# Kernel tuning notes

Measured on AMD Instinct MI355X. Metric: run time of the kernel, lower is better.

The kernel has to match this reference:

```python
import jax, jax.numpy as jnp
import numpy as np

B, S, H, L, NH, DH, FF = 64, 256, 768, 12, 12, 64, 3072
V, MAXP, NTYPE, NI, NS = 30522, 512, 2, 10, 64


def setup_inputs() -> dict:
    key = jax.random.key(0)
    ks = iter(jax.random.split(key, 40))
    n = lambda shp, s=0.02: jax.random.normal(next(ks), shp, jnp.float32) * s
    inp = {
        'input_ids': jax.random.randint(next(ks), (B, S), 0, V),
        'attention_mask': jnp.ones((B, S), jnp.int32),
        'token_type_ids': jnp.zeros((B, S), jnp.int32),
        'intent_labels': jax.random.randint(next(ks), (B,), 0, NI),
        'slot_labels': jax.random.randint(next(ks), (B, S), 0, NS),
        'word_emb': n((V, H)), 'pos_emb': n((MAXP, H)), 'type_emb': n((NTYPE, H)),
        'emb_ln_g': jnp.ones((H,)), 'emb_ln_b': jnp.zeros((H,)),
        'Wq': n((L, H, H)), 'bq': jnp.zeros((L, H)),
        'Wk': n((L, H, H)), 'bk': jnp.zeros((L, H)),
        'Wv': n((L, H, H)), 'bv': jnp.zeros((L, H)),
        'Wo': n((L, H, H)), 'bo': jnp.zeros((L, H)),
        'ln1_g': jnp.ones((L, H)), 'ln1_b': jnp.zeros((L, H)),
        'W1': n((L, H, FF)), 'b1': jnp.zeros((L, FF)),
        'W2': n((L, FF, H)), 'b2': jnp.zeros((L, H)),
        'ln2_g': jnp.ones((L, H)), 'ln2_b': jnp.zeros((L, H)),
        'Wi': n((H, NI)), 'bi': jnp.zeros((NI,)),
        'Ws': n((H, NS)), 'bs': jnp.zeros((NS,)),
        'crf_start': n((NS,), 0.1), 'crf_end': n((NS,), 0.1),
        'crf_trans': n((NS, NS), 0.1),
    }
    return inp


def _ln(x, g, b):
    m = x.mean(-1, keepdims=True)
    v = jnp.square(x - m).mean(-1, keepdims=True)
    return (x - m) * jax.lax.rsqrt(v + 1e-12) * g + b


def _forward(params, input_ids, attention_mask, token_type_ids, intent_labels, slot_labels):
    (word_emb, pos_emb, type_emb, emb_ln_g, emb_ln_b,
     Wq, bq, Wk, bk, Wv, bv, Wo, bo, ln1_g, ln1_b,
     W1, b1, W2, b2, ln2_g, ln2_b,
     Wi, bi, Ws, bs, crf_start, crf_end, crf_trans) = params
    Bn, Sn = input_ids.shape
    Hn = word_emb.shape[1]
    dh = Hn // NH
    # BERT embeddings (dropout is identity in eval)
    x = word_emb[input_ids] + pos_emb[:Sn][None] + type_emb[token_type_ids]
    x = _ln(x, emb_ln_g, emb_ln_b)
    bias = (1.0 - attention_mask.astype(x.dtype))[:, None, None, :] * -1e9  # [B,1,1,S]

    def layer(h, p):
        wq, cq, wk, ck, wv, cv, wo, co, g1, d1, w1, e1, w2, e2, g2, d2 = p
        q = (h @ wq + cq).reshape(Bn, Sn, NH, dh)
        k = (h @ wk + ck).reshape(Bn, Sn, NH, dh)
        v = (h @ wv + cv).reshape(Bn, Sn, NH, dh)
        sc = jnp.einsum('bqnd,bknd->bnqk', q, k) / jnp.sqrt(jnp.float32(dh)) + bias
        a = jax.nn.softmax(sc, axis=-1)
        ctx = jnp.einsum('bnqk,bknd->bqnd', a, v).reshape(Bn, Sn, Hn)
        h2 = _ln(h + ctx @ wo + co, g1, d1)
        ff = jax.nn.gelu(h2 @ w1 + e1, approximate=False)
        return _ln(h2 + ff @ w2 + e2, g2, d2), None

    x, _ = jax.lax.scan(layer, x, (Wq, bq, Wk, bk, Wv, bv, Wo, bo,
                                   ln1_g, ln1_b, W1, b1, W2, b2, ln2_g, ln2_b))
    intent_logits = x[:, 0, :] @ Wi + bi           # [B, NI]
    slot_logits = x @ Ws + bs                      # [B, S, NS]
    # intent cross-entropy (mean over batch)
    lp = jax.nn.log_softmax(intent_logits, axis=-1)
    intent_loss = -jnp.take_along_axis(lp, intent_labels[:, None], axis=1).mean()
    # CRF log-likelihood
    mask = attention_mask.astype(slot_logits.dtype)
    em, tags = slot_logits, slot_labels
    t0 = tags[:, 0]
    score = crf_start[t0] + jnp.take_along_axis(em[:, 0, :], t0[:, None], axis=1)[:, 0]
    prev, cur = tags[:, :-1], tags[:, 1:]
    step_sc = crf_trans[prev, cur] + jnp.take_along_axis(em[:, 1:, :], cur[..., None], axis=2)[..., 0]
    score = score + (step_sc * mask[:, 1:]).sum(1)
    lengths = attention_mask.sum(1)
    last_tag = jnp.take_along_axis(tags, (lengths - 1)[:, None].astype(tags.dtype), axis=1)[:, 0]
    score = score + crf_end[last_tag]
    em_t = jnp.swapaxes(em, 0, 1)    # [S,B,C]
    mk_t = jnp.swapaxes(mask, 0, 1)  # [S,B]
    alpha0 = crf_start[None, :] + em_t[0]

    def crf_step(alpha, xs):
        e, m = xs
        nxt = jax.scipy.special.logsumexp(alpha[:, :, None] + crf_trans[None], axis=1) + e
        return jnp.where(m[:, None] > 0, nxt, alpha), None

    alpha, _ = jax.lax.scan(crf_step, alpha0, (em_t[1:], mk_t[1:]))
    logZ = jax.scipy.special.logsumexp(alpha + crf_end[None, :], axis=1)
    llh = score - logZ                # per-sequence log-likelihood
    crf_loss = -llh.mean()
    return intent_loss + 2.0 * crf_loss


def reference(input_ids, attention_mask, token_type_ids, intent_labels, slot_labels,
              word_emb, pos_emb, type_emb, emb_ln_g, emb_ln_b,
              Wq, bq, Wk, bk, Wv, bv, Wo, bo, ln1_g, ln1_b,
              W1, b1, W2, b2, ln2_g, ln2_b,
              Wi, bi, Ws, bs, crf_start, crf_end, crf_trans):
    params = (word_emb, pos_emb, type_emb, emb_ln_g, emb_ln_b,
              Wq, bq, Wk, bk, Wv, bv, Wo, bo, ln1_g, ln1_b,
              W1, b1, W2, b2, ln2_g, ln2_b,
              Wi, bi, Ws, bs, crf_start, crf_end, crf_trans)
    return _forward(params, input_ids, attention_mask, token_type_ids, intent_labels, slot_labels)
```

## Files before the change

kernel.cpp:

```cpp
#include <hip/hip_runtime.h>
#include <stdint.h>

typedef unsigned short u16;
typedef __attribute__((ext_vector_type(8))) short bh8;
typedef __attribute__((ext_vector_type(4))) float f4;
typedef __attribute__((ext_vector_type(4))) short s4v;

#define DEV static __device__ __forceinline__

DEV u16 f2bf(float f){ union{float f; uint32_t u;} v; v.f=f; uint32_t r=v.u + 0x7FFFu + ((v.u>>16)&1u); return (u16)(r>>16); }
DEV float bf2f(u16 u){ union{uint32_t u; float f;} v; v.u=((uint32_t)u)<<16; return v.f; }

DEV void mfma16(f4& d, bh8 a, bh8 b){
  d = __builtin_amdgcn_mfma_f32_16x16x32_bf16(a, b, d, 0, 0, 0);
}

DEV float gelu(float v){
  float x = v*0.70710678118f;
  float ax = fabsf(x);
  float tt = 1.0f/(1.0f + 0.3275911f*ax);
  float y = 1.0f - (((((1.061405429f*tt - 1.453152027f)*tt) + 1.421413741f)*tt
                     - 0.284496736f)*tt + 0.254829592f)*tt*__expf(-ax*ax);
  float e = (x<0.f)? -y : y;
  return 0.5f*v*(1.0f+e);
}

#define GLD16(g,l) __builtin_amdgcn_global_load_lds( \
    (__attribute__((address_space(1))) void*)(void*)(g), \
    (__attribute__((address_space(3))) void*)(void*)(l), 16, 0, 0)

struct GemmP { const u16* A; const u16* B; int K; void* C; int ldc;
               const float* b0; const float* b1; const float* b2; const u16* res; };

template<int EPI>
DEV void epi_store(const GemmP& p, int gr, int gc, float v){
  if(EPI==0){
    const float* bp = (gc<768)? p.b0 : (gc<1536? p.b1 : p.b2);
    const int bc = (gc<768)? gc : (gc<1536? gc-768 : gc-1536);
    ((u16*)p.C)[(size_t)gr*p.ldc + gc] = f2bf(v + bp[bc]);
  } else if(EPI==1){
    v += p.b0[gc] + bf2f(p.res[(size_t)gr*p.ldc + gc]);
    ((u16*)p.C)[(size_t)gr*p.ldc + gc] = f2bf(v);
  } else if(EPI==2){
    ((u16*)p.C)[(size_t)gr*p.ldc + gc] = f2bf(gelu(v + p.b0[gc]));
  } else {
    v += (gc<64)? p.b0[gc] : 0.f;
    ((float*)p.C)[(size_t)gr*p.ldc + gc] = v;
  }
}

template<int EPI>
__global__ __launch_bounds__(512)
void gemm256(GemmP p){
  extern __shared__ char smem[];
  const int t=threadIdx.x, l=t&63, w=t>>6;
  const int wr=w>>2, wc=w&3;
  const int m0=blockIdx.x*256, n0=blockIdx.y*256;
  const int K=p.K, NT=K>>6;
  const int fl=l&15, fh=l>>4;

  const int r0=(w*1024+l*16)>>7;
  const int cs=(((l&7)^(l>>3))<<4);
  const char* gA0 = (const char*)p.A + ((size_t)(m0+r0)*K)*2 + cs;
  const char* gB0 = (const char*)p.B + ((size_t)(n0+r0)*K)*2 + cs;
  const size_t rowblk = (size_t)64*K*2;
  char* dA = smem + w*1024;
  char* dB = smem + 32768 + w*1024;

  #define SG_A(T,h,buf) do{ const char* _s=gA0 + (size_t)(T)*128 + (size_t)(h)*2*rowblk; \
    char* _d=dA+(buf)*65536+(h)*16384; GLD16(_s,_d); GLD16(_s+rowblk,_d+8192); }while(0)
  #define SG_B(T,h,buf) do{ const char* _s=gB0 + (size_t)(T)*128 + (size_t)(h)*2*rowblk; \
    char* _d=dB+(buf)*65536+(h)*16384; GLD16(_s,_d); GLD16(_s+rowblk,_d+8192); }while(0)

  int oB[4][2], oA[8][2];
#pragma unroll
  for(int nf=0;nf<4;nf++){ const int rw=wc*64+nf*16+fl;
#pragma unroll
    for(int ks=0;ks<2;ks++) oB[nf][ks] = 32768 + rw*128 + ((ks*64+fh*16) ^ ((rw&7)<<4)); }
#pragma unroll
  for(int mf=0;mf<8;mf++){ const int rw=wr*128+mf*16+fl;
#pragma unroll
    for(int ks=0;ks<2;ks++) oA[mf][ks] = rw*128 + ((ks*64+fh*16) ^ ((rw&7)<<4)); }

  f4 acc[8][4] = {};

  SG_A(0,0,0); SG_A(0,1,0); SG_B(0,0,0); SG_B(0,1,0);
  if(NT>1){ SG_B(1,0,1); SG_B(1,1,1);
            asm volatile("s_waitcnt vmcnt(4)":::"memory"); }
  else    { asm volatile("s_waitcnt vmcnt(0)":::"memory"); }
  __syncthreads();

  for(int T=0; T<NT; ++T){
    const int cur=T&1;
    const char* sb = smem + (cur<<16);
    if(T+1<NT){ SG_A(T+1,0,cur^1); SG_A(T+1,1,cur^1); }
    bh8 bf[4][2], af[2][2];
#pragma unroll
    for(int nf=0;nf<4;nf++){ bf[nf][0]=*(const bh8*)(sb+oB[nf][0]); bf[nf][1]=*(const bh8*)(sb+oB[nf][1]); }
    af[0][0]=*(const bh8*)(sb+oA[0][0]); af[0][1]=*(const bh8*)(sb+oA[0][1]);
    af[1][0]=*(const bh8*)(sb+oA[1][0]); af[1][1]=*(const bh8*)(sb+oA[1][1]);
#pragma unroll
    for(int j=0;j<2;j++)
#pragma unroll
      for(int nf=0;nf<4;nf++){ mfma16(acc[j][nf], af[j][0], bf[nf][0]); mfma16(acc[j][nf], af[j][1], bf[nf][1]); }
    __syncthreads();
    if(T+2<NT){ SG_B(T+2,0,cur); SG_B(T+2,1,cur); }
    af[0][0]=*(const bh8*)(sb+oA[2][0]); af[0][1]=*(const bh8*)(sb+oA[2][1]);
    af[1][0]=*(const bh8*)(sb+oA[3][0]); af[1][1]=*(const bh8*)(sb+oA[3][1]);
#pragma unroll
    for(int j=0;j<2;j++)
#pragma unroll
      for(int nf=0;nf<4;nf++){ mfma16(acc[2+j][nf], af[j][0], bf[nf][0]); mfma16(acc[2+j][nf], af[j][1], bf[nf][1]); }
    af[0][0]=*(const bh8*)(sb+oA[4][0]); af[0][1]=*(const bh8*)(sb+oA[4][1]);
    af[1][0]=*(const bh8*)(sb+oA[5][0]); af[1][1]=*(const bh8*)(sb+oA[5][1]);
#pragma unroll
    for(int j=0;j<2;j++)
#pragma unroll
      for(int nf=0;nf<4;nf++){ mfma16(acc[4+j][nf], af[j][0], bf[nf][0]); mfma16(acc[4+j][nf], af[j][1], bf[nf][1]); }
    af[0][0]=*(const bh8*)(sb+oA[6][0]); af[0][1]=*(const bh8*)(sb+oA[6][1]);
    af[1][0]=*(const bh8*)(sb+oA[7][0]); af[1][1]=*(const bh8*)(sb+oA[7][1]);
#pragma unroll
    for(int j=0;j<2;j++)
#pragma unroll
      for(int nf=0;nf<4;nf++){ mfma16(acc[6+j][nf], af[j][0], bf[nf][0]); mfma16(acc[6+j][nf], af[j][1], bf[nf][1]); }
    if(T+2<NT)      asm volatile("s_waitcnt vmcnt(4)":::"memory");
    else if(T+1<NT) asm volatile("s_waitcnt vmcnt(0)":::"memory");
    __syncthreads();
  }
  #undef SG_A
  #undef SG_B

  const int lr=fh*4;
#pragma unroll
  for(int m=0;m<8;m++)
#pragma unroll
  for(int n=0;n<4;n++)
#pragma unroll
  for(int r=0;r<4;r++){
    epi_store<EPI>(p, m0 + wr*128 + m*16 + lr + r, n0 + wc*64 + n*16 + fl, acc[m][n][r]);
  }
}

template<int EPI>
__global__ __launch_bounds__(256)
void gemm128(GemmP p){
  __shared__ __align__(16) u16 As[128*32];
  __shared__ __align__(16) u16 Bs[128*32];
  const int t=threadIdx.x, l=t&63, w=t>>6, wr=w>>1, wc=w&1;
  const int fl=l&15, fh=l>>4;
  const int m0=blockIdx.x*128, n0=blockIdx.y*128;
  const int K=p.K, NT=K>>5;
  const int srow = t>>2;
  const int cs = (((t&3) ^ (srow&3))<<4);
  const char* gA = (const char*)p.A + ((size_t)(m0+srow)*K)*2 + cs;
  const char* gB = (const char*)p.B + ((size_t)(n0+srow)*K)*2 + cs;
  const size_t r64 = (size_t)64*K*2;
  char* dA = (char*)As + t*16;
  char* dB = (char*)Bs + t*16;

  int oA2[4], oB2[4];
#pragma unroll
  for(int mf=0;mf<4;mf++){ const int rw=wr*64+mf*16+fl;
    oA2[mf] = rw*64 + ((fh ^ (rw&3))<<4); }
#pragma unroll
  for(int nf=0;nf<4;nf++){ const int rw=wc*64+nf*16+fl;
    oB2[nf] = rw*64 + ((fh ^ (rw&3))<<4); }

  f4 acc[4][4] = {};
  for(int T=0; T<NT; ++T){
    GLD16(gA + (size_t)T*64, dA);
    GLD16(gA + (size_t)T*64 + r64, dA + 4096);
    GLD16(gB + (size_t)T*64, dB);
    GLD16(gB + (size_t)T*64 + r64, dB + 4096);
    __syncthreads();
    bh8 af[4], bfr[4];
#pragma unroll
    for(int mf=0;mf<4;mf++) af[mf]=*(const bh8*)((const char*)As+oA2[mf]);
#pragma unroll
    for(int nf=0;nf<4;nf++) bfr[nf]=*(const bh8*)((const char*)Bs+oB2[nf]);
#pragma unroll
    for(int m=0;m<4;m++)
#pragma unroll
      for(int n=0;n<4;n++) mfma16(acc[m][n], af[m], bfr[n]);
    __syncthreads();
  }
  const int lr=fh*4;
#pragma unroll
  for(int m=0;m<4;m++)
#pragma unroll
  for(int n=0;n<4;n++)
#pragma unroll
  for(int r=0;r<4;r++){
    epi_store<EPI>(p, m0 + wr*64 + m*16 + lr + r, n0 + wc*64 + n*16 + fl, acc[m][n][r]);
  }
}

__global__ __launch_bounds__(256)
void attn_kernel(const u16* __restrict__ qkv, const int* __restrict__ amask, u16* __restrict__ ctx){
  __shared__ __align__(16) u16 Ks[256*64];
  __shared__ __align__(16) u16 Vt[64*256];
  __shared__ __align__(16) u16 Ps[4*64*64];
  __shared__ float biasS[256];
  const int t=threadIdx.x, l=t&63, w=t>>6;
  const int b=blockIdx.x/12, h=blockIdx.x%12;
  biasS[t] = (1.f - (float)amask[b*256+t]) * -1e9f;
  const u16* kb = qkv + ((size_t)b*256)*2304 + 768 + h*64;
  const u16* vb = kb + 768;
#pragma unroll
  for(int i=0;i<8;i++){
    const int c = t + i*256;
    const int row = c>>3, seg = c&7;
    uint4 kv = *(const uint4*)(kb + (size_t)row*2304 + seg*8);
    const int ba = row*128 + seg*16;
    *(uint4*)((char*)Ks + (ba ^ ((row&7)<<4))) = kv;
    uint4 vv = *(const uint4*)(vb + (size_t)row*2304 + seg*8);
    const u16* pv = (const u16*)&vv;
#pragma unroll
    for(int j=0;j<8;j++){
      const int d = seg*8+j;
      const int bb = d*512 + row*2;
      *(u16*)((char*)Vt + (bb ^ ((d&7)<<4))) = pv[j];
    }
  }
  bh8 aq[4][2];
  const u16* qb = qkv + ((size_t)b*256 + w*64)*2304 + h*64;
#pragma unroll
  for(int m=0;m<4;m++)
#pragma unroll
    for(int ks=0;ks<2;ks++)
      aq[m][ks] = *(const bh8*)(qb + (size_t)(m*16+(l&15))*2304 + ks*32 + (l>>4)*8);
  __syncthreads();
  float mrun[4][4], lrun[4][4];
  f4 o[4][4] = {};
#pragma unroll
  for(int m=0;m<4;m++)
#pragma unroll
    for(int r=0;r<4;r++){ mrun[m][r] = -3e38f; lrun[m][r]=0.f; }
  u16* Pw = Ps + w*4096;
  for(int kt=0;kt<4;kt++){
    f4 sacc[4][4] = {};
#pragma unroll
    for(int ks=0;ks<2;ks++)
#pragma unroll
      for(int n=0;n<4;n++){
        const int row = kt*64 + n*16 + (l&15);
        const int by = row*128 + ks*64 + (l>>4)*16;
        bh8 bk = *(const bh8*)((const char*)Ks + (by ^ ((row&7)<<4)));
#pragma unroll
        for(int m=0;m<4;m++) mfma16(sacc[m][n], aq[m][ks], bk);
      }
#pragma unroll
    for(int m=0;m<4;m++){
      float rmax[4] = {-3e38f,-3e38f,-3e38f,-3e38f};
#pragma unroll
      for(int n=0;n<4;n++){
        const float bi = biasS[kt*64 + n*16 + (l&15)];
#pragma unroll
        for(int r=0;r<4;r++){
          float sv = sacc[m][n][r]*0.125f + bi;
          sacc[m][n][r] = sv;
          rmax[r] = fmaxf(rmax[r], sv);
        }
      }
#pragma unroll
      for(int dd=1; dd<16; dd<<=1)
#pragma unroll
        for(int r=0;r<4;r++) rmax[r] = fmaxf(rmax[r], __shfl_xor(rmax[r], dd));
      float psum[4];
#pragma unroll
      for(int r=0;r<4;r++){
        const float mn = fmaxf(mrun[m][r], rmax[r]);
        const float corr = __expf(mrun[m][r] - mn);
        mrun[m][r] = mn;
        lrun[m][r] *= corr;
#pragma unroll
        for(int nd=0; nd<4; nd++) o[m][nd][r] *= corr;
        psum[r] = 0.f;
      }
#pragma unroll
      for(int n=0;n<4;n++)
#pragma unroll
        for(int r=0;r<4;r++){
          const float pvv = __expf(sacc[m][n][r] - mrun[m][r]);
          sacc[m][n][r] = pvv;
          psum[r] += pvv;
        }
#pragma unroll
      for(int dd=1; dd<16; dd<<=1)
#pragma unroll
        for(int r=0;r<4;r++) psum[r] += __shfl_xor(psum[r], dd);
#pragma unroll
      for(int r=0;r<4;r++) lrun[m][r] += psum[r];
#pragma unroll
      for(int n=0;n<4;n++)
#pragma unroll
        for(int r=0;r<4;r++){
          const int prow = m*16 + (l>>4)*4 + r;
          const int pcol = n*16 + (l&15);
          const int by = prow*128 + pcol*2;
          *(u16*)((char*)Pw + (by ^ ((prow&7)<<4))) = f2bf(sacc[m][n][r]);
        }
    }
#pragma unroll
    for(int ks=0;ks<2;ks++){
      bh8 ap[4];
#pragma unroll
      for(int m=0;m<4;m++){
        const int prow = m*16 + (l&15);
        const int by = prow*128 + (ks*32 + (l>>4)*8)*2;
        ap[m] = *(const bh8*)((const char*)Pw + (by ^ ((prow&7)<<4)));
      }
#pragma unroll
      for(int nd=0; nd<4; nd++){
        const int dR = nd*16 + (l&15);
        const int by = dR*512 + (kt*64 + ks*32 + (l>>4)*8)*2;
        bh8 bv = *(const bh8*)((const char*)Vt + (by ^ ((dR&7)<<4)));
#pragma unroll
        for(int m=0;m<4;m++) mfma16(o[m][nd], ap[m], bv);
      }
    }
  }
#pragma unroll
  for(int m=0;m<4;m++)
#pragma unroll
  for(int nd=0; nd<4; nd++)
#pragma unroll
  for(int r=0;r<4;r++){
    const int row = w*64 + m*16 + (l>>4)*4 + r;
    const float vv = o[m][nd][r] / lrun[m][r];
    ctx[((size_t)b*256 + row)*768 + h*64 + nd*16 + (l&15)] = f2bf(vv);
  }
}

__global__ void ln_kernel(const u16* __restrict__ in, const float* __restrict__ g,
                          const float* __restrict__ b, u16* __restrict__ out){
  const int row = blockIdx.x, t = threadIdx.x;
  __shared__ float red[8];
  const bool act = t < 192;
  float v0=0,v1=0,v2=0,v3=0;
  if(act){
    s4v x = *(const s4v*)(in + (size_t)row*768 + t*4);
    v0=bf2f((u16)x[0]); v1=bf2f((u16)x[1]); v2=bf2f((u16)x[2]); v3=bf2f((u16)x[3]);
  }
  float s = (v0+v1)+(v2+v3);
  float q = (v0*v0+v1*v1)+(v2*v2+v3*v3);
#pragma unroll
  for(int dd=1; dd<64; dd<<=1){ s += __shfl_xor(s,dd); q += __shfl_xor(q,dd); }
  if((t&63)==0){ red[t>>6]=s; red[4+(t>>6)]=q; }
  __syncthreads();
  s = red[0]+red[1]+red[2];
  q = red[4]+red[5]+red[6];
  const float mean = s*(1.f/768.f);
  float var = q*(1.f/768.f) - mean*mean; var = fmaxf(var, 0.f);
  const float rs = rsqrtf(var + 1e-12f);
  if(act){
    float4 gv = *(const float4*)(g + t*4);
    float4 bv = *(const float4*)(b + t*4);
    s4v o;
    o[0]=(short)f2bf((v0-mean)*rs*gv.x + bv.x);
    o[1]=(short)f2bf((v1-mean)*rs*gv.y + bv.y);
    o[2]=(short)f2bf((v2-mean)*rs*gv.z + bv.z);
    o[3]=(short)f2bf((v3-mean)*rs*gv.w + bv.w);
    *(s4v*)(out + (size_t)row*768 + t*4) = o;
  }
}

__global__ void embed_ln(const int* __restrict__ ids, const int* __restrict__ tti,
    const float* __restrict__ we, const float* __restrict__ pe, const float* __restrict__ te,
    const float* __restrict__ g, const float* __restrict__ bb, u16* __restrict__ x){
  const int tok = blockIdx.x, t = threadIdx.x;
  __shared__ float red[8];
  const int id = ids[tok], tyid = tti[tok], s0 = tok & 255;
  const bool act = t < 192;
  float v0=0,v1=0,v2=0,v3=0;
  if(act){
    float4 a = *(const float4*)(we + (size_t)id*768 + t*4);
    float4 pp = *(const float4*)(pe + (size_t)s0*768 + t*4);
    float4 ty = *(const float4*)(te + (size_t)tyid*768 + t*4);
    v0=a.x+pp.x+ty.x; v1=a.y+pp.y+ty.y; v2=a.z+pp.z+ty.z; v3=a.w+pp.w+ty.w;
  }
  float s = (v0+v1)+(v2+v3);
  float q = (v0*v0+v1*v1)+(v2*v2+v3*v3);
#pragma unroll
  for(int dd=1; dd<64; dd<<=1){ s += __shfl_xor(s,dd); q += __shfl_xor(q,dd); }
  if((t&63)==0){ red[t>>6]=s; red[4+(t>>6)]=q; }
  __syncthreads();
  s = red[0]+red[1]+red[2];
  q = red[4]+red[5]+red[6];
  const float mean = s*(1.f/768.f);
  float var = q*(1.f/768.f) - mean*mean; var = fmaxf(var, 0.f);
  const float rs = rsqrtf(var + 1e-12f);
  if(act){
    float4 gv = *(const float4*)(g + t*4);
    float4 bv = *(const float4*)(bb + t*4);
    s4v o;
    o[0]=(short)f2bf((v0-mean)*rs*gv.x + bv.x);
    o[1]=(short)f2bf((v1-mean)*rs*gv.y + bv.y);
    o[2]=(short)f2bf((v2-mean)*rs*gv.z + bv.z);
    o[3]=(short)f2bf((v3-mean)*rs*gv.w + bv.w);
    *(s4v*)(x + (size_t)tok*768 + t*4) = o;
  }
}

__global__ void transpose_cvt(const float* __restrict__ src, u16* __restrict__ dst, int R, int C){
  __shared__ float sm[32][33];
  const int ntc = C>>5;
  const int tr = blockIdx.x/ntc, tc = blockIdx.x - tr*ntc;
  const int r0 = tr<<5, c0 = tc<<5;
  const int tx = threadIdx.x, ty2 = threadIdx.y;
#pragma unroll
  for(int i=0;i<4;i++) sm[ty2+i*8][tx] = src[(size_t)(r0+ty2+i*8)*C + c0+tx];
  __syncthreads();
#pragma unroll
  for(int i=0;i<4;i++) dst[(size_t)(c0+ty2+i*8)*R + r0+tx] = f2bf(sm[tx][ty2+i*8]);
}

__global__ void conv_layer(const float* __restrict__ Wq, const float* __restrict__ Wk,
    const float* __restrict__ Wv, const float* __restrict__ Wo,
    const float* __restrict__ W1, const float* __restrict__ W2, u16* __restrict__ Wt){
  __shared__ float sm[32][33];
  const int bid = blockIdx.x;
  const float* src; u16* dst; int R, C, tt;
  if(bid<2304){
    R=768; C=768; const int mi = bid/576; tt = bid - mi*576;
    src = (mi==0?Wq: mi==1?Wk: mi==2?Wv: Wo);
    dst = Wt + (size_t)mi*589824;
  } else if(bid<4608){ R=768; C=3072; tt=bid-2304; src=W1; dst=Wt+2359296; }
  else { R=3072; C=768; tt=bid-4608; src=W2; dst=Wt+4718592; }
  const int ntc=C>>5; const int tr=tt/ntc, tc=tt-tr*ntc;
  const int r0=tr<<5, c0=tc<<5, tx=threadIdx.x, ty2=threadIdx.y;
#pragma unroll
  for(int i=0;i<4;i++) sm[ty2+i*8][tx] = src[(size_t)(r0+ty2+i*8)*C + c0+tx];
  __syncthreads();
#pragma unroll
  for(int i=0;i<4;i++) dst[(size_t)(c0+ty2+i*8)*R + r0+tx] = f2bf(sm[tx][ty2+i*8]);
}

__global__ void intent_kernel(const u16* __restrict__ x, const float* __restrict__ Wi,
    const float* __restrict__ bi, const int* __restrict__ lab, float* __restrict__ parts){
  const int b = blockIdx.x, t = threadIdx.x;
  __shared__ float xs[768];
  __shared__ float lg[10];
  const u16* rp = x + ((size_t)b*256)*768;
#pragma unroll
  for(int i=0;i<3;i++) xs[t+i*256] = bf2f(rp[t+i*256]);
  __syncthreads();
  if(t<10){
    float s = bi[t];
    for(int k=0;k<768;k++) s += xs[k]*Wi[(size_t)k*10 + t];
    lg[t] = s;
  }
  __syncthreads();
  if(t==0){
    float m = lg[0];
    for(int j=1;j<10;j++) m = fmaxf(m, lg[j]);
    float se = 0.f;
    for(int j=0;j<10;j++) se += expf(lg[j]-m);
    parts[b] = (logf(se) + m) - lg[lab[b]];
  }
}

__global__ __launch_bounds__(64)
void crf_kernel(const float* __restrict__ em, const int* __restrict__ tags,
    const int* __restrict__ amask, const float* __restrict__ cs, const float* __restrict__ ce,
    const float* __restrict__ tr, float* __restrict__ parts){
  const int b = blockIdx.x, j = threadIdx.x;
  const float* eb = em + (size_t)b*256*128;
  const int* tg = tags + b*256;
  const int* mk = amask + b*256;
  __shared__ __align__(16) float aS[64];
  float Etr[64];
#pragma unroll
  for(int i=0;i<64;i++) Etr[i] = __expf(tr[i*64 + j]);
  float sc = 0.f; int len = 0;
  for(int s=j+1; s<256; s+=64){
    const int pv = tg[s-1], cu = tg[s];
    sc += (tr[pv*64+cu] + eb[(size_t)s*128+cu]) * (float)mk[s];
  }
  for(int s=j; s<256; s+=64) len += mk[s];
#pragma unroll
  for(int dd=1; dd<64; dd<<=1){ sc += __shfl_xor(sc,dd); len += __shfl_xor(len,dd); }
  const int t0 = tg[0];
  float score = sc + cs[t0] + eb[t0] + ce[tg[len-1]];
  float a = __expf(cs[j] + eb[j]);
  float logc = 0.f;
  float em_s = eb[128 + j];
  int   mk_s = mk[1];
  for(int s=1; s<256; s++){
    const int sn = (s<255)? s+1 : s;
    const float em_n = eb[(size_t)sn*128 + j];
    const int   mk_n = mk[sn];
    aS[j] = a;
    __syncthreads();
    float acc0=0.f, acc1=0.f, acc2=0.f, acc3=0.f;
    const float4* ap = (const float4*)aS;
#pragma unroll
    for(int q2=0;q2<16;q2++){
      const float4 av = ap[q2];
      acc0 += av.x*Etr[4*q2+0];
      acc1 += av.y*Etr[4*q2+1];
      acc2 += av.z*Etr[4*q2+2];
      acc3 += av.w*Etr[4*q2+3];
    }
    __syncthreads();
    const float nxt = ((acc0+acc1)+(acc2+acc3)) * __expf(em_s);
    a = (mk_s > 0) ? nxt : a;
    if((s&7)==7){
      const float c = __shfl(a, 0);
      logc += __logf(c);
      a *= (1.f/c);
    }
    em_s = em_n; mk_s = mk_n;
  }
  float v2 = logf(a) + logc + ce[j];
  float am2 = v2;
#pragma unroll
  for(int dd=1; dd<64; dd<<=1) am2 = fmaxf(am2, __shfl_xor(am2,dd));
  float se = __expf(v2 - am2);
#pragma unroll
  for(int dd=1; dd<64; dd<<=1) se += __shfl_xor(se,dd);
  if(j==0) parts[64+b] = (logf(se)+am2) - score;
}

__global__ void final_reduce(const float* __restrict__ parts, float* __restrict__ out){
  const int t = threadIdx.x;
  float a = parts[t], c = parts[64+t];
#pragma unroll
  for(int dd=1; dd<64; dd<<=1){ a += __shfl_xor(a,dd); c += __shfl_xor(c,dd); }
  if(t==0) out[0] = a*(1.f/64.f) + 2.f*c*(1.f/64.f);
}

extern "C" void kernel_launch(void* const* d_in, const int* in_sizes, int n_in,
                              void* d_out, int out_size, void* d_ws, size_t ws_size,
                              hipStream_t stream){
  (void)in_sizes; (void)n_in; (void)out_size;
  const int* ids   = (const int*)d_in[0];
  const int* amask = (const int*)d_in[1];
  const int* tti   = (const int*)d_in[2];
  const int* ilab  = (const int*)d_in[3];
  const int* slab  = (const int*)d_in[4];
  const float* we  = (const float*)d_in[5];
  const float* pe  = (const float*)d_in[6];
  const float* te  = (const float*)d_in[7];
  const float* eg  = (const float*)d_in[8];
  const float* ebt = (const float*)d_in[9];
  const float* Wq  = (const float*)d_in[10];
  const float* bq  = (const float*)d_in[11];
  const float* Wk  = (const float*)d_in[12];
  const float* bkk = (const float*)d_in[13];
  const float* Wv  = (const float*)d_in[14];
  const float* bvv = (const float*)d_in[15];
  const float* Wo  = (const float*)d_in[16];
  const float* bo  = (const float*)d_in[17];
  const float* l1g = (const float*)d_in[18];
  const float* l1b = (const float*)d_in[19];
  const float* W1  = (const float*)d_in[20];
  const float* b1  = (const float*)d_in[21];
  const float* W2  = (const float*)d_in[22];
  const float* b2  = (const float*)d_in[23];
  const float* l2g = (const float*)d_in[24];
  const float* l2b = (const float*)d_in[25];
  const float* Wi  = (const float*)d_in[26];
  const float* bi  = (const float*)d_in[27];
  const float* Wsp = (const float*)d_in[28];
  const float* bs  = (const float*)d_in[29];
  const float* cs  = (const float*)d_in[30];
  const float* ce  = (const float*)d_in[31];
  const float* ctr = (const float*)d_in[32];

  char* ws = (char*)d_ws;
  size_t off = 0;
  auto alloc = [&](size_t bytes)->void*{ void* p = ws + off; off += (bytes+255)&~(size_t)255; return p; };
  u16* x     = (u16*)alloc(16384ull*768*2);
  u16* h2    = (u16*)alloc(16384ull*768*2);
  u16* y     = (u16*)alloc(16384ull*768*2);
  u16* qkv   = (u16*)alloc(16384ull*2304*2);
  u16* cf    = (u16*)alloc(16384ull*3072*2);
  u16* Wt    = (u16*)alloc(7077888ull*2);
  u16* WsT   = (u16*)alloc(128ull*768*2);
  float* slots = (float*)alloc(16384ull*128*4);
  float* parts = (float*)alloc(512);
  if(off > ws_size) return;

  (void)hipFuncSetAttribute((const void*)gemm256<0>, hipFuncAttributeMaxDynamicSharedMemorySize, 131072);
  (void)hipFuncSetAttribute((const void*)gemm256<2>, hipFuncAttributeMaxDynamicSharedMemorySize, 131072);

  dim3 T256(256), T512(512), T328(32,8);
  embed_ln<<<dim3(16384), T256, 0, stream>>>(ids, tti, we, pe, te, eg, ebt, x);
  transpose_cvt<<<dim3(48), T328, 0, stream>>>(Wsp, WsT, 768, 64);
  for(int L=0; L<12; L++){
    const size_t oH = (size_t)L*768*768, oF = (size_t)L*768*3072;
    conv_layer<<<dim3(6912), T328, 0, stream>>>(Wq+oH, Wk+oH, Wv+oH, Wo+oH, W1+oF, W2+oF, Wt);
    GemmP pq{ x, Wt, 768, qkv, 2304, bq+L*768, bkk+L*768, bvv+L*768, nullptr };
    gemm256<0><<<dim3(64,9), T512, 131072, stream>>>(pq);
    attn_kernel<<<dim3(768), T256, 0, stream>>>(qkv, amask, cf);
    GemmP po{ cf, Wt+1769472, 768, y, 768, bo+L*768, nullptr, nullptr, x };
    gemm128<1><<<dim3(128,6), T256, 0, stream>>>(po);
    ln_kernel<<<dim3(16384), T256, 0, stream>>>(y, l1g+L*768, l1b+L*768, h2);
    GemmP p1{ h2, Wt+2359296, 768, cf, 3072, b1+L*3072, nullptr, nullptr, nullptr };
    gemm256<2><<<dim3(64,12), T512, 131072, stream>>>(p1);
    GemmP p2{ cf, Wt+4718592, 3072, y, 768, b2+L*768, nullptr, nullptr, h2 };
    gemm128<1><<<dim3(128,6), T256, 0, stream>>>(p2);
    ln_kernel<<<dim3(16384), T256, 0, stream>>>(y, l2g+L*768, l2b+L*768, x);
  }
  GemmP psl{ x, WsT, 768, slots, 128, bs, nullptr, nullptr, nullptr };
  gemm128<3><<<dim3(128,1), T256, 0, stream>>>(psl);
  intent_kernel<<<dim3(64), T256, 0, stream>>>(x, Wi, bi, ilab, parts);
  crf_kernel<<<dim3(64), dim3(64), 0, stream>>>(slots, slab, amask, cs, ce, ctr, parts);
  final_reduce<<<dim3(1), dim3(64), 0, stream>>>(parts, (float*)d_out);
}
```

Baseline: 5.687 ms.

## Replace 256-tile GEMM with 128-tile GEMM and fix LDS swizzle

Removes the double-buffered 256x256 GEMM kernel and runs the QKV and FFN1 projections through the simpler 128x128 single-buffered kernel with more blocks. The LDS XOR swizzle in the 128 kernel is changed to key on row bits 1-2 instead of 0-1, intended to reduce bank conflicts on fragment reads. This trades the larger tile's data reuse and load/compute overlap for higher occupancy and more blocks, and risks more global traffic and exposed load latency.

```diff
diff --git a/kernel.cpp b/kernel.cpp
--- a/kernel.cpp
+++ b/kernel.cpp
@@ -50,98 +50,6 @@
 }
 
 template<int EPI>
-__global__ __launch_bounds__(512)
-void gemm256(GemmP p){
-  extern __shared__ char smem[];
-  const int t=threadIdx.x, l=t&63, w=t>>6;
-  const int wr=w>>2, wc=w&3;
-  const int m0=blockIdx.x*256, n0=blockIdx.y*256;
-  const int K=p.K, NT=K>>6;
-  const int fl=l&15, fh=l>>4;
-
-  const int r0=(w*1024+l*16)>>7;
-  const int cs=(((l&7)^(l>>3))<<4);
-  const char* gA0 = (const char*)p.A + ((size_t)(m0+r0)*K)*2 + cs;
-  const char* gB0 = (const char*)p.B + ((size_t)(n0+r0)*K)*2 + cs;
-  const size_t rowblk = (size_t)64*K*2;
-  char* dA = smem + w*1024;
-  char* dB = smem + 32768 + w*1024;
-
-  #define SG_A(T,h,buf) do{ const char* _s=gA0 + (size_t)(T)*128 + (size_t)(h)*2*rowblk; \
-    char* _d=dA+(buf)*65536+(h)*16384; GLD16(_s,_d); GLD16(_s+rowblk,_d+8192); }while(0)
-  #define SG_B(T,h,buf) do{ const char* _s=gB0 + (size_t)(T)*128 + (size_t)(h)*2*rowblk; \
-    char* _d=dB+(buf)*65536+(h)*16384; GLD16(_s,_d); GLD16(_s+rowblk,_d+8192); }while(0)
-
-  int oB[4][2], oA[8][2];
-#pragma unroll
-  for(int nf=0;nf<4;nf++){ const int rw=wc*64+nf*16+fl;
-#pragma unroll
-    for(int ks=0;ks<2;ks++) oB[nf][ks] = 32768 + rw*128 + ((ks*64+fh*16) ^ ((rw&7)<<4)); }
-#pragma unroll
-  for(int mf=0;mf<8;mf++){ const int rw=wr*128+mf*16+fl;
-#pragma unroll
-    for(int ks=0;ks<2;ks++) oA[mf][ks] = rw*128 + ((ks*64+fh*16) ^ ((rw&7)<<4)); }
-
-  f4 acc[8][4] = {};
-
-  SG_A(0,0,0); SG_A(0,1,0); SG_B(0,0,0); SG_B(0,1,0);
-  if(NT>1){ SG_B(1,0,1); SG_B(1,1,1);
-            asm volatile("s_waitcnt vmcnt(4)":::"memory"); }
-  else    { asm volatile("s_waitcnt vmcnt(0)":::"memory"); }
-  __syncthreads();
-
-  for(int T=0; T<NT; ++T){
-    const int cur=T&1;
-    const char* sb = smem + (cur<<16);
-    if(T+1<NT){ SG_A(T+1,0,cur^1); SG_A(T+1,1,cur^1); }
-    bh8 bf[4][2], af[2][2];
-#pragma unroll
-    for(int nf=0;nf<4;nf++){ bf[nf][0]=*(const bh8*)(sb+oB[nf][0]); bf[nf][1]=*(const bh8*)(sb+oB[nf][1]); }
-    af[0][0]=*(const bh8*)(sb+oA[0][0]); af[0][1]=*(const bh8*)(sb+oA[0][1]);
-    af[1][0]=*(const bh8*)(sb+oA[1][0]); af[1][1]=*(const bh8*)(sb+oA[1][1]);
-#pragma unroll
-    for(int j=0;j<2;j++)
-#pragma unroll
-      for(int nf=0;nf<4;nf++){ mfma16(acc[j][nf], af[j][0], bf[nf][0]); mfma16(acc[j][nf], af[j][1], bf[nf][1]); }
-    __syncthreads();
-    if(T+2<NT){ SG_B(T+2,0,cur); SG_B(T+2,1,cur); }
-    af[0][0]=*(const bh8*)(sb+oA[2][0]); af[0][1]=*(const bh8*)(sb+oA[2][1]);
-    af[1][0]=*(const bh8*)(sb+oA[3][0]); af[1][1]=*(const bh8*)(sb+oA[3][1]);
-#pragma unroll
-    for(int j=0;j<2;j++)
-#pragma unroll
-      for(int nf=0;nf<4;nf++){ mfma16(acc[2+j][nf], af[j][0], bf[nf][0]); mfma16(acc[2+j][nf], af[j][1], bf[nf][1]); }
-    af[0][0]=*(const bh8*)(sb+oA[4][0]); af[0][1]=*(const bh8*)(sb+oA[4][1]);
-    af[1][0]=*(const bh8*)(sb+oA[5][0]); af[1][1]=*(const bh8*)(sb+oA[5][1]);
-#pragma unroll
-    for(int j=0;j<2;j++)
-#pragma unroll
-      for(int nf=0;nf<4;nf++){ mfma16(acc[4+j][nf], af[j][0], bf[nf][0]); mfma16(acc[4+j][nf], af[j][1], bf[nf][1]); }
-    af[0][0]=*(const bh8*)(sb+oA[6][0]); af[0][1]=*(const bh8*)(sb+oA[6][1]);
-    af[1][0]=*(const bh8*)(sb+oA[7][0]); af[1][1]=*(const bh8*)(sb+oA[7][1]);
-#pragma unroll
-    for(int j=0;j<2;j++)
-#pragma unroll
-      for(int nf=0;nf<4;nf++){ mfma16(acc[6+j][nf], af[j][0], bf[nf][0]); mfma16(acc[6+j][nf], af[j][1], bf[nf][1]); }
-    if(T+2<NT)      asm volatile("s_waitcnt vmcnt(4)":::"memory");
-    else if(T+1<NT) asm volatile("s_waitcnt vmcnt(0)":::"memory");
-    __syncthreads();
-  }
-  #undef SG_A
-  #undef SG_B
-
-  const int lr=fh*4;
-#pragma unroll
-  for(int m=0;m<8;m++)
-#pragma unroll
-  for(int n=0;n<4;n++)
-#pragma unroll
-  for(int r=0;r<4;r++){
-    epi_store<EPI>(p, m0 + wr*128 + m*16 + lr + r, n0 + wc*64 + n*16 + fl, acc[m][n][r]);
-  }
-}
-
-template<int EPI>
 __global__ __launch_bounds__(256)
 void gemm128(GemmP p){
   __shared__ __align__(16) u16 As[128*32];
@@ -151,7 +59,7 @@
   const int m0=blockIdx.x*128, n0=blockIdx.y*128;
   const int K=p.K, NT=K>>5;
   const int srow = t>>2;
-  const int cs = (((t&3) ^ (srow&3))<<4);
+  const int cs = (((t&3) ^ ((t>>3)&3))<<4);
   const char* gA = (const char*)p.A + ((size_t)(m0+srow)*K)*2 + cs;
   const char* gB = (const char*)p.B + ((size_t)(n0+srow)*K)*2 + cs;
   const size_t r64 = (size_t)64*K*2;
@@ -161,10 +69,10 @@
   int oA2[4], oB2[4];
 #pragma unroll
   for(int mf=0;mf<4;mf++){ const int rw=wr*64+mf*16+fl;
-    oA2[mf] = rw*64 + ((fh ^ (rw&3))<<4); }
+    oA2[mf] = rw*64 + ((fh ^ ((rw>>1)&3))<<4); }
 #pragma unroll
   for(int nf=0;nf<4;nf++){ const int rw=wc*64+nf*16+fl;
-    oB2[nf] = rw*64 + ((fh ^ (rw&3))<<4); }
+    oB2[nf] = rw*64 + ((fh ^ ((rw>>1)&3))<<4); }
 
   f4 acc[4][4] = {};
   for(int T=0; T<NT; ++T){
@@ -582,23 +490,20 @@
   float* parts = (float*)alloc(512);
   if(off > ws_size) return;
 
-  (void)hipFuncSetAttribute((const void*)gemm256<0>, hipFuncAttributeMaxDynamicSharedMemorySize, 131072);
-  (void)hipFuncSetAttribute((const void*)gemm256<2>, hipFuncAttributeMaxDynamicSharedMemorySize, 131072);
-
-  dim3 T256(256), T512(512), T328(32,8);
+  dim3 T256(256), T328(32,8);
   embed_ln<<<dim3(16384), T256, 0, stream>>>(ids, tti, we, pe, te, eg, ebt, x);
   transpose_cvt<<<dim3(48), T328, 0, stream>>>(Wsp, WsT, 768, 64);
   for(int L=0; L<12; L++){
     const size_t oH = (size_t)L*768*768, oF = (size_t)L*768*3072;
     conv_layer<<<dim3(6912), T328, 0, stream>>>(Wq+oH, Wk+oH, Wv+oH, Wo+oH, W1+oF, W2+oF, Wt);
     GemmP pq{ x, Wt, 768, qkv, 2304, bq+L*768, bkk+L*768, bvv+L*768, nullptr };
-    gemm256<0><<<dim3(64,9), T512, 131072, stream>>>(pq);
+    gemm128<0><<<dim3(128,18), T256, 0, stream>>>(pq);
     attn_kernel<<<dim3(768), T256, 0, stream>>>(qkv, amask, cf);
     GemmP po{ cf, Wt+1769472, 768, y, 768, bo+L*768, nullptr, nullptr, x };
     gemm128<1><<<dim3(128,6), T256, 0, stream>>>(po);
     ln_kernel<<<dim3(16384), T256, 0, stream>>>(y, l1g+L*768, l1b+L*768, h2);
     GemmP p1{ h2, Wt+2359296, 768, cf, 3072, b1+L*3072, nullptr, nullptr, nullptr };
-    gemm256<2><<<dim3(64,12), T512, 131072, stream>>>(p1);
+    gemm128<2><<<dim3(128,24), T256, 0, stream>>>(p1);
     GemmP p2{ cf, Wt+4718592, 3072, y, 768, b2+L*768, nullptr, nullptr, h2 };
     gemm128<1><<<dim3(128,6), T256, 0, stream>>>(p2);
     ln_kernel<<<dim3(16384), T256, 0, stream>>>(y, l2g+L*768, l2b+L*768, x);
```

New measurement: 6.227 ms. +9.5%, slower.
